# Performance work log

Measured on AMD Instinct MI355X. Metric: run time of the kernel, lower is better.

The kernel has to match this reference:

```python
import jax, jax.numpy as jnp
import numpy as np

D_MODEL = 1024
NHEAD = 16
HEAD_DIM = D_MODEL // NHEAD
EPS = 1e-5


def layer_norm(x, gamma, beta):
    mu = jnp.mean(x, axis=-1, keepdims=True)
    var = jnp.mean(jnp.square(x - mu), axis=-1, keepdims=True)
    return (x - mu) * jax.lax.rsqrt(var + EPS) * gamma + beta


def setup_inputs() -> dict:
    key = jax.random.key(0)
    ks = jax.random.split(key, 12)
    d = D_MODEL
    s = 1.0 / np.sqrt(d)
    return {
        "x": jax.random.normal(ks[0], (4, 2048, d), dtype=jnp.float32),
        "wq": jax.random.normal(ks[1], (d, d), dtype=jnp.float32) * s,
        "wk": jax.random.normal(ks[2], (d, d), dtype=jnp.float32) * s,
        "wv": jax.random.normal(ks[3], (d, d), dtype=jnp.float32) * s,
        "wo": jax.random.normal(ks[4], (d, d), dtype=jnp.float32) * s,
        "bo": jnp.zeros((d,), dtype=jnp.float32),
        "gx": jnp.ones((d,), dtype=jnp.float32),
        "bx": jnp.zeros((d,), dtype=jnp.float32),
        "gf": jnp.ones((d,), dtype=jnp.float32),
        "bf": jnp.zeros((d,), dtype=jnp.float32),
        "w1": jax.random.normal(ks[5], (d, d), dtype=jnp.float32) * s,
        "b1": jnp.zeros((d,), dtype=jnp.float32),
        "w2": jax.random.normal(ks[6], (d, d), dtype=jnp.float32) * s,
        "b2": jnp.zeros((d,), dtype=jnp.float32),
    }


def reference(x, wq, wk, wv, wo, bo, gx, bx, gf, bf, w1, b1, w2, b2):
    B, S, D = x.shape
    H, Dh = NHEAD, HEAD_DIM
    xs = layer_norm(x, gx, bx)
    q = (xs @ wq).reshape(B, S, H, Dh)
    k = (xs @ wk).reshape(B, S, H, Dh)
    v = (xs @ wv).reshape(B, S, H, Dh)
    scores = jnp.einsum("bqhd,bkhd->bhqk", q, k) / jnp.sqrt(jnp.float32(Dh))
    attn = jax.nn.softmax(scores, axis=-1)  # dropout p=0 -> identity
    o = jnp.einsum("bhqk,bkhd->bqhd", attn, v).reshape(B, S, D)
    attn_out = o @ wo + bo
    xt = x + attn_out
    h = layer_norm(xt, gf, bf)
    ffn = jax.nn.relu(h @ w1 + b1) @ w2 + b2
    return xt + ffn
```

## Files before the change

### kernel.cpp

```cpp
#include <hip/hip_runtime.h>
#include <hip/hip_bf16.h>

typedef __bf16 bf16;
typedef bf16 bf16x8 __attribute__((ext_vector_type(8)));
typedef bf16 bf16x4 __attribute__((ext_vector_type(4)));
typedef float f32x4 __attribute__((ext_vector_type(4)));
typedef float f32x16 __attribute__((ext_vector_type(16)));

#define AS1 __attribute__((address_space(1)))
#define AS3 __attribute__((address_space(3)))

static constexpr int SEQ = 2048;
static constexpr int NH  = 16;
static constexpr int DH  = 64;
static constexpr float SCLQ = 0.125f * 1.44269504088896340736f;

__device__ __forceinline__ void gload16(const void* g, void* l) {
  __builtin_amdgcn_global_load_lds((const AS1 void*)g, (AS3 void*)l, 16, 0, 0);
}

__device__ __forceinline__ unsigned pk2(float a, float b) {
  union { bf16 h[2]; unsigned u; } z;
  z.h[0] = (bf16)a; z.h[1] = (bf16)b;
  return z.u;
}

__device__ __forceinline__ void plswap(unsigned &a, unsigned &b) {
  asm volatile("v_permlane32_swap_b32 %0, %1" : "+v"(a), "+v"(b));
}

#define MFMA32(d, a, b) d = __builtin_amdgcn_mfma_f32_32x32x16_bf16(a, b, d, 0, 0, 0)

__global__ __launch_bounds__(256) void prep_w(
    const float* __restrict__ w0, const float* __restrict__ w1,
    const float* __restrict__ w2, const float* __restrict__ w3,
    const float* __restrict__ w4, const float* __restrict__ w5,
    bf16* __restrict__ dst)
{
  __shared__ float tile[64][65];
  int bid = blockIdx.x;
  int wi = bid >> 8;
  int tl = bid & 255;
  int tk = (tl >> 4) << 6;
  int tn = (tl & 15) << 6;
  const float* W = w0;
  if (wi == 1) W = w1; else if (wi == 2) W = w2; else if (wi == 3) W = w3;
  else if (wi == 4) W = w4; else if (wi == 5) W = w5;
  int t = threadIdx.x;
  #pragma unroll
  for (int rep = 0; rep < 16; ++rep) {
    int idx = rep * 256 + t;
    int i = idx >> 6, j = idx & 63;
    tile[i][j] = W[(size_t)(tk + i) * 1024 + tn + j];
  }
  __syncthreads();
  bf16* out = dst + (size_t)wi * 1024 * 1024;
  #pragma unroll
  for (int rep = 0; rep < 16; ++rep) {
    int idx = rep * 256 + t;
    int i = idx >> 6, j = idx & 63;
    out[(size_t)(tn + i) * 1024 + tk + j] = (bf16)tile[j][i];
  }
}

__global__ __launch_bounds__(256) void ln_k(
    const float* __restrict__ x, const float* __restrict__ g,
    const float* __restrict__ bb, bf16* __restrict__ out)
{
  int row = blockIdx.x;
  int t = threadIdx.x;
  float4 v = ((const float4*)(x + (size_t)row * 1024))[t];
  float s  = v.x + v.y + v.z + v.w;
  float s2 = v.x * v.x + v.y * v.y + v.z * v.z + v.w * v.w;
  #pragma unroll
  for (int m = 1; m < 64; m <<= 1) { s += __shfl_xor(s, m); s2 += __shfl_xor(s2, m); }
  __shared__ float red[8];
  int w = t >> 6;
  if ((t & 63) == 0) { red[w] = s; red[4 + w] = s2; }
  __syncthreads();
  s  = red[0] + red[1] + red[2] + red[3];
  s2 = red[4] + red[5] + red[6] + red[7];
  float mu  = s * (1.0f / 1024.0f);
  float var = s2 * (1.0f / 1024.0f) - mu * mu;
  float rst = rsqrtf(var + 1e-5f);
  float4 gv = ((const float4*)g)[t];
  float4 bv = ((const float4*)bb)[t];
  bf16x4 o;
  o[0] = (bf16)((v.x - mu) * rst * gv.x + bv.x);
  o[1] = (bf16)((v.y - mu) * rst * gv.y + bv.y);
  o[2] = (bf16)((v.z - mu) * rst * gv.z + bv.z);
  o[3] = (bf16)((v.w - mu) * rst * gv.w + bv.w);
  *(bf16x4*)(out + (size_t)row * 1024 + t * 4) = o;
}

template<int EPI, int NT>
__global__ __launch_bounds__(256) void gemm_k(
    const bf16* __restrict__ A, const bf16* __restrict__ Bt,
    const float* __restrict__ bias, const float* __restrict__ res,
    float* __restrict__ outf, bf16* __restrict__ outb)
{
  __shared__ bf16 lA[128 * 64];
  __shared__ bf16 lB[128 * 64];
  int t = threadIdx.x;
  int wg = blockIdx.x;
  int swz = (wg & 7) * (NT * 8) + (wg >> 3);
  int mt = swz / NT, nt = swz % NT;
  int lane = t & 63, w = t >> 6;
  int l16 = lane & 15, lh = lane >> 4;
  int wr = w >> 1, wc = w & 1;

  f32x4 acc[4][4] = {};
  const size_t mbase = (size_t)mt * 128;
  const size_t nbase = (size_t)nt * 128;
  int u = t & 7;

  for (int ks = 0; ks < 16; ++ks) {
    int k0 = ks * 64;
    #pragma unroll
    for (int i = 0; i < 4; ++i) {
      int row = i * 32 + (t >> 3);
      int up = u ^ (row & 7);
      gload16(A  + (mbase + row) * 1024 + k0 + up * 8, lA + i * 2048 + w * 512);
      gload16(Bt + (nbase + row) * 1024 + k0 + up * 8, lB + i * 2048 + w * 512);
    }
    __syncthreads();
    #pragma unroll
    for (int kc = 0; kc < 2; ++kc) {
      bf16x8 af[4], bfr[4];
      #pragma unroll
      for (int mi = 0; mi < 4; ++mi) {
        int row = wr * 64 + mi * 16 + l16;
        af[mi] = *(const bf16x8*)(lA + row * 64 + (((kc * 4 + lh) ^ (row & 7)) * 8));
      }
      #pragma unroll
      for (int ni = 0; ni < 4; ++ni) {
        int row = wc * 64 + ni * 16 + l16;
        bfr[ni] = *(const bf16x8*)(lB + row * 64 + (((kc * 4 + lh) ^ (row & 7)) * 8));
      }
      #pragma unroll
      for (int mi = 0; mi < 4; ++mi)
        #pragma unroll
        for (int ni = 0; ni < 4; ++ni)
          acc[mi][ni] = __builtin_amdgcn_mfma_f32_16x16x32_bf16(af[mi], bfr[ni], acc[mi][ni], 0, 0, 0);
    }
    __syncthreads();
  }

  int mrow0 = mt * 128 + wr * 64;
  int ncol0 = nt * 128 + wc * 64;
  #pragma unroll
  for (int mi = 0; mi < 4; ++mi) {
    #pragma unroll
    for (int ni = 0; ni < 4; ++ni) {
      if constexpr (EPI == 0) {
        int gcol = ncol0 + ni * 16 + l16;
        int which = gcol >> 10;
        int col = gcol & 1023;
        int h = col >> 6, dh = col & 63;
        bf16* dst = outb + (size_t)which * (size_t)(4 * NH * SEQ * DH);
        if (which == 2) {
          int s0 = mrow0 + mi * 16 + lh * 4;
          int b = s0 >> 11, s = s0 & 2047;
          bf16x4 pkv;
          #pragma unroll
          for (int r = 0; r < 4; ++r) pkv[r] = (bf16)acc[mi][ni][r];
          *(bf16x4*)(dst + (((size_t)((b * NH + h) * DH + dh)) << 11) + s) = pkv;
        } else {
          #pragma unroll
          for (int r = 0; r < 4; ++r) {
            int grow = mrow0 + mi * 16 + lh * 4 + r;
            int b = grow >> 11, s = grow & 2047;
            float v = acc[mi][ni][r];
            if (which == 0) v *= SCLQ;
            dst[(((size_t)((b * NH + h) * SEQ + s)) << 6) + dh] = (bf16)v;
          }
        }
      } else {
        #pragma unroll
        for (int r = 0; r < 4; ++r) {
          int grow = mrow0 + mi * 16 + lh * 4 + r;
          int gcol = ncol0 + ni * 16 + l16;
          float v = acc[mi][ni][r];
          if constexpr (EPI == 2) {
            size_t idx = (size_t)grow * 1024 + gcol;
            outf[idx] = v + bias[gcol] + res[idx];
          } else {
            size_t idx = (size_t)grow * 1024 + gcol;
            float z = v + bias[gcol];
            outb[idx] = (bf16)(z > 0.f ? z : 0.f);
          }
        }
      }
    }
  }
}

__global__ __launch_bounds__(256, 2) void attn_k(
    const bf16* __restrict__ q, const bf16* __restrict__ kk,
    const bf16* __restrict__ vt, bf16* __restrict__ o)
{
  __shared__ bf16 lK[2][4096];
  __shared__ bf16 lV[2][4096];

  int t = threadIdx.x;
  int lane = t & 63, w = t >> 6;
  int l31 = lane & 31, hi = lane >> 5;
  int bid = blockIdx.x;
  int swz = (bid & 7) * 64 + (bid >> 3);
  int bh = swz >> 3, qt = swz & 7;
  int q0 = qt * 256 + w * 64;
  size_t bhS = (size_t)bh * SEQ;

  const bf16* qrow0 = q + (bhS + q0 + l31) * 64 + hi * 8;
  const bf16* qrow1 = qrow0 + 32 * 64;
  bf16x8 aq0[4], aq1[4];
  #pragma unroll
  for (int ks = 0; ks < 4; ++ks) {
    aq0[ks] = *(const bf16x8*)(qrow0 + ks * 16);
    aq1[ks] = *(const bf16x8*)(qrow1 + ks * 16);
  }

  int srow = t >> 3;
  int u8 = (t & 7) ^ (srow & 7);
  const bf16* kSrc = kk + (bhS + srow) * 64 + u8 * 8;
  const bf16* vSrc = vt + ((size_t)bh * 64 + srow) * SEQ + u8 * 8;

  f32x16 oa00 = {}, oa01 = {}, oa10 = {}, oa11 = {};
  float lsum0 = 0.f, lsum1 = 0.f;

  gload16(kSrc,            &lK[0][w * 512]);
  gload16(kSrc + 2048,     &lK[0][2048 + w * 512]);
  gload16(vSrc,            &lV[0][w * 512]);
  gload16(vSrc + 32 * SEQ, &lV[0][2048 + w * 512]);
  __syncthreads();

  #pragma unroll 2
  for (int kt = 0; kt < 32; ++kt) {
    const int cur = kt & 1;
    if (kt < 31) {
      const bf16* ks2 = kSrc + (size_t)(kt + 1) * 4096;
      const bf16* vs2 = vSrc + (kt + 1) * 64;
      gload16(ks2,            &lK[cur ^ 1][w * 512]);
      gload16(ks2 + 2048,     &lK[cur ^ 1][2048 + w * 512]);
      gload16(vs2,            &lV[cur ^ 1][w * 512]);
      gload16(vs2 + 32 * SEQ, &lV[cur ^ 1][2048 + w * 512]);
    }

    const bf16* bK = &lK[cur][0];
    const bf16* bV = &lV[cur][0];

    f32x16 sA0 = {}, sB0 = {}, sA1 = {}, sB1 = {};
    __builtin_amdgcn_s_setprio(1);
    #pragma unroll
    for (int ks = 0; ks < 4; ++ks) {
      int u = ((2 * ks + hi) ^ (l31 & 7)) * 8;
      bf16x8 k0 = *(const bf16x8*)(bK + l31 * 64 + u);
      bf16x8 k1 = *(const bf16x8*)(bK + (32 + l31) * 64 + u);
      MFMA32(sA0, k0, aq0[ks]);
      MFMA32(sA1, k0, aq1[ks]);
      MFMA32(sB0, k1, aq0[ks]);
      MFMA32(sB1, k1, aq1[ks]);
    }
    __builtin_amdgcn_s_setprio(0);

    unsigned cv0[4][4], cv1[4][4];
    {
      float p[32];
      #pragma unroll
      for (int i = 0; i < 16; ++i) {
        p[i]      = __builtin_amdgcn_exp2f(sA0[i]);
        p[16 + i] = __builtin_amdgcn_exp2f(sB0[i]);
      }
      float t8[8];
      #pragma unroll
      for (int i = 0; i < 8; ++i)
        t8[i] = (p[4 * i] + p[4 * i + 1]) + (p[4 * i + 2] + p[4 * i + 3]);
      lsum0 += ((t8[0] + t8[1]) + (t8[2] + t8[3])) + ((t8[4] + t8[5]) + (t8[6] + t8[7]));
      #pragma unroll
      for (int ks = 0; ks < 4; ++ks) {
        int g = 8 * ks;
        unsigned X0 = pk2(p[g],     p[g + 1]), X1 = pk2(p[g + 2], p[g + 3]);
        unsigned Y0 = pk2(p[g + 4], p[g + 5]), Y1 = pk2(p[g + 6], p[g + 7]);
        plswap(X0, Y0);
        plswap(X1, Y1);
        cv0[ks][0] = X0; cv0[ks][1] = X1; cv0[ks][2] = Y0; cv0[ks][3] = Y1;
      }
    }
    {
      float p[32];
      #pragma unroll
      for (int i = 0; i < 16; ++i) {
        p[i]      = __builtin_amdgcn_exp2f(sA1[i]);
        p[16 + i] = __builtin_amdgcn_exp2f(sB1[i]);
      }
      float t8[8];
      #pragma unroll
      for (int i = 0; i < 8; ++i)
        t8[i] = (p[4 * i] + p[4 * i + 1]) + (p[4 * i + 2] + p[4 * i + 3]);
      lsum1 += ((t8[0] + t8[1]) + (t8[2] + t8[3])) + ((t8[4] + t8[5]) + (t8[6] + t8[7]));
      #pragma unroll
      for (int ks = 0; ks < 4; ++ks) {
        int g = 8 * ks;
        unsigned X0 = pk2(p[g],     p[g + 1]), X1 = pk2(p[g + 2], p[g + 3]);
        unsigned Y0 = pk2(p[g + 4], p[g + 5]), Y1 = pk2(p[g + 6], p[g + 7]);
        plswap(X0, Y0);
        plswap(X1, Y1);
        cv1[ks][0] = X0; cv1[ks][1] = X1; cv1[ks][2] = Y0; cv1[ks][3] = Y1;
      }
    }

    __builtin_amdgcn_s_setprio(1);
    #pragma unroll
    for (int ks = 0; ks < 4; ++ks) {
      int u = ((2 * ks + hi) ^ (l31 & 7)) * 8;
      bf16x8 v0 = *(const bf16x8*)(bV + l31 * 64 + u);
      bf16x8 v1 = *(const bf16x8*)(bV + (32 + l31) * 64 + u);
      union { unsigned u4[4]; bf16x8 v; } a0, a1;
      a0.u4[0] = cv0[ks][0]; a0.u4[1] = cv0[ks][1]; a0.u4[2] = cv0[ks][2]; a0.u4[3] = cv0[ks][3];
      a1.u4[0] = cv1[ks][0]; a1.u4[1] = cv1[ks][1]; a1.u4[2] = cv1[ks][2]; a1.u4[3] = cv1[ks][3];
      MFMA32(oa00, a0.v, v0);
      MFMA32(oa01, a0.v, v1);
      MFMA32(oa10, a1.v, v0);
      MFMA32(oa11, a1.v, v1);
    }
    __builtin_amdgcn_s_setprio(0);

    __syncthreads();
  }

  lsum0 += __shfl_xor(lsum0, 32);
  lsum1 += __shfl_xor(lsum1, 32);
  float inv0 = 1.0f / lsum0;
  float inv1 = 1.0f / lsum1;
  int bb = bh >> 4, hh = bh & 15;
  size_t obase = ((size_t)bb * SEQ + q0) * 1024 + (size_t)hh * 64;
  #pragma unroll
  for (int r = 0; r < 16; ++r) {
    int qrw = (r & 3) + 8 * (r >> 2) + 4 * hi;
    float iv0 = __shfl(inv0, qrw);
    float iv1 = __shfl(inv1, qrw);
    size_t b0 = obase + (size_t)qrw * 1024;
    size_t b1 = obase + (size_t)(32 + qrw) * 1024;
    o[b0 + l31]      = (bf16)(oa00[r] * iv0);
    o[b0 + 32 + l31] = (bf16)(oa01[r] * iv0);
    o[b1 + l31]      = (bf16)(oa10[r] * iv1);
    o[b1 + 32 + l31] = (bf16)(oa11[r] * iv1);
  }
}

extern "C" void kernel_launch(void* const* d_in, const int* in_sizes, int n_in,
                              void* d_out, int out_size, void* d_ws, size_t ws_size,
                              hipStream_t stream) {
  const float* x   = (const float*)d_in[0];
  const float* wq  = (const float*)d_in[1];
  const float* wk  = (const float*)d_in[2];
  const float* wv  = (const float*)d_in[3];
  const float* wo  = (const float*)d_in[4];
  const float* bo  = (const float*)d_in[5];
  const float* gx  = (const float*)d_in[6];
  const float* bx  = (const float*)d_in[7];
  const float* gf  = (const float*)d_in[8];
  const float* bfp = (const float*)d_in[9];
  const float* w1  = (const float*)d_in[10];
  const float* b1  = (const float*)d_in[11];
  const float* w2  = (const float*)d_in[12];
  const float* b2  = (const float*)d_in[13];

  char* ws = (char*)d_ws;
  const size_t MB = 1024 * 1024;
  bf16*  wT  = (bf16*)ws;
  bf16*  xs  = (bf16*)(ws + 12 * MB);
  bf16*  qb  = (bf16*)(ws + 28 * MB);
  bf16*  kb  = (bf16*)(ws + 44 * MB);
  bf16*  vtb = (bf16*)(ws + 60 * MB);
  bf16*  ob  = (bf16*)(ws + 12 * MB);
  float* xt  = (float*)(ws + 28 * MB);
  bf16*  hb  = (bf16*)(ws + 60 * MB);
  bf16*  a1  = (bf16*)(ws + 12 * MB);
  float* out = (float*)d_out;

  prep_w<<<1536, 256, 0, stream>>>(wq, wk, wv, wo, w1, w2, wT);
  ln_k<<<8192, 256, 0, stream>>>(x, gx, bx, xs);
  gemm_k<0, 24><<<1536, 256, 0, stream>>>(xs, wT, nullptr, nullptr, nullptr, qb);
  attn_k<<<512, 256, 0, stream>>>(qb, kb, vtb, ob);
  gemm_k<2, 8><<<512, 256, 0, stream>>>(ob, wT + (size_t)3 * MB, bo, x, xt, nullptr);
  ln_k<<<8192, 256, 0, stream>>>(xt, gf, bfp, hb);
  gemm_k<3, 8><<<512, 256, 0, stream>>>(hb, wT + (size_t)4 * MB, b1, nullptr, nullptr, a1);
  gemm_k<2, 8><<<512, 256, 0, stream>>>(a1, wT + (size_t)5 * MB, b2, xt, out, nullptr);
}
```

Baseline: 271.4 us.

## Fuse weight prep with first layernorm and store residual xt as bf16

Merges the weight transpose/convert kernel and the first layernorm into one launch, with block ranges split by blockIdx, which saves a kernel launch and lets the two independent jobs overlap. The intermediate residual xt is now stored in bf16 instead of fp32. This halves its write traffic and the reads by the second layernorm and the final GEMM epilogue. In exchange the residual path loses precision, which may raise the final output error.

Result: faster. 264.1 us (-2.7%).

```diff
diff --git a/kernel.cpp b/kernel.cpp
--- a/kernel.cpp
+++ b/kernel.cpp
@@ -31,22 +31,53 @@
 
 #define MFMA32(d, a, b) d = __builtin_amdgcn_mfma_f32_32x32x16_bf16(a, b, d, 0, 0, 0)
 
-__global__ __launch_bounds__(256) void prep_w(
+__global__ __launch_bounds__(256) void prep_ln(
     const float* __restrict__ w0, const float* __restrict__ w1,
     const float* __restrict__ w2, const float* __restrict__ w3,
     const float* __restrict__ w4, const float* __restrict__ w5,
-    bf16* __restrict__ dst)
+    bf16* __restrict__ dst,
+    const float* __restrict__ x, const float* __restrict__ g,
+    const float* __restrict__ bb, bf16* __restrict__ xs)
 {
   __shared__ float tile[64][65];
+  __shared__ float red[8];
   int bid = blockIdx.x;
-  int wi = bid >> 8;
-  int tl = bid & 255;
+  int t = threadIdx.x;
+
+  if (bid < 8192) {
+    int row = bid;
+    float4 v = ((const float4*)(x + (size_t)row * 1024))[t];
+    float s  = v.x + v.y + v.z + v.w;
+    float s2 = v.x * v.x + v.y * v.y + v.z * v.z + v.w * v.w;
+    #pragma unroll
+    for (int m = 1; m < 64; m <<= 1) { s += __shfl_xor(s, m); s2 += __shfl_xor(s2, m); }
+    int w = t >> 6;
+    if ((t & 63) == 0) { red[w] = s; red[4 + w] = s2; }
+    __syncthreads();
+    s  = red[0] + red[1] + red[2] + red[3];
+    s2 = red[4] + red[5] + red[6] + red[7];
+    float mu  = s * (1.0f / 1024.0f);
+    float var = s2 * (1.0f / 1024.0f) - mu * mu;
+    float rst = rsqrtf(var + 1e-5f);
+    float4 gv = ((const float4*)g)[t];
+    float4 bv = ((const float4*)bb)[t];
+    bf16x4 o;
+    o[0] = (bf16)((v.x - mu) * rst * gv.x + bv.x);
+    o[1] = (bf16)((v.y - mu) * rst * gv.y + bv.y);
+    o[2] = (bf16)((v.z - mu) * rst * gv.z + bv.z);
+    o[3] = (bf16)((v.w - mu) * rst * gv.w + bv.w);
+    *(bf16x4*)(xs + (size_t)row * 1024 + t * 4) = o;
+    return;
+  }
+
+  int pb = bid - 8192;
+  int wi = pb >> 8;
+  int tl = pb & 255;
   int tk = (tl >> 4) << 6;
   int tn = (tl & 15) << 6;
   const float* W = w0;
   if (wi == 1) W = w1; else if (wi == 2) W = w2; else if (wi == 3) W = w3;
   else if (wi == 4) W = w4; else if (wi == 5) W = w5;
-  int t = threadIdx.x;
   #pragma unroll
   for (int rep = 0; rep < 16; ++rep) {
     int idx = rep * 256 + t;
@@ -63,13 +94,20 @@
   }
 }
 
+template<int BF>
 __global__ __launch_bounds__(256) void ln_k(
-    const float* __restrict__ x, const float* __restrict__ g,
+    const void* __restrict__ xin, const float* __restrict__ g,
     const float* __restrict__ bb, bf16* __restrict__ out)
 {
   int row = blockIdx.x;
   int t = threadIdx.x;
-  float4 v = ((const float4*)(x + (size_t)row * 1024))[t];
+  float4 v;
+  if constexpr (BF) {
+    bf16x4 h = ((const bf16x4*)((const bf16*)xin + (size_t)row * 1024))[t];
+    v.x = (float)h[0]; v.y = (float)h[1]; v.z = (float)h[2]; v.w = (float)h[3];
+  } else {
+    v = ((const float4*)((const float*)xin + (size_t)row * 1024))[t];
+  }
   float s  = v.x + v.y + v.z + v.w;
   float s2 = v.x * v.x + v.y * v.y + v.z * v.z + v.w * v.w;
   #pragma unroll
@@ -96,7 +134,8 @@
 template<int EPI, int NT>
 __global__ __launch_bounds__(256) void gemm_k(
     const bf16* __restrict__ A, const bf16* __restrict__ Bt,
-    const float* __restrict__ bias, const float* __restrict__ res,
+    const float* __restrict__ bias, const float* __restrict__ resf,
+    const bf16* __restrict__ resb,
     float* __restrict__ outf, bf16* __restrict__ outb)
 {
   __shared__ bf16 lA[128 * 64];
@@ -181,13 +220,14 @@
           int grow = mrow0 + mi * 16 + lh * 4 + r;
           int gcol = ncol0 + ni * 16 + l16;
           float v = acc[mi][ni][r];
+          size_t idx = (size_t)grow * 1024 + gcol;
           if constexpr (EPI == 2) {
-            size_t idx = (size_t)grow * 1024 + gcol;
-            outf[idx] = v + bias[gcol] + res[idx];
-          } else {
-            size_t idx = (size_t)grow * 1024 + gcol;
+            outb[idx] = (bf16)(v + bias[gcol] + resf[idx]);
+          } else if constexpr (EPI == 3) {
             float z = v + bias[gcol];
             outb[idx] = (bf16)(z > 0.f ? z : 0.f);
+          } else {
+            outf[idx] = v + bias[gcol] + (float)resb[idx];
           }
         }
       }
@@ -374,17 +414,16 @@
   bf16*  kb  = (bf16*)(ws + 44 * MB);
   bf16*  vtb = (bf16*)(ws + 60 * MB);
   bf16*  ob  = (bf16*)(ws + 12 * MB);
-  float* xt  = (float*)(ws + 28 * MB);
+  bf16*  xtb = (bf16*)(ws + 28 * MB);
   bf16*  hb  = (bf16*)(ws + 60 * MB);
   bf16*  a1  = (bf16*)(ws + 12 * MB);
   float* out = (float*)d_out;
 
-  prep_w<<<1536, 256, 0, stream>>>(wq, wk, wv, wo, w1, w2, wT);
-  ln_k<<<8192, 256, 0, stream>>>(x, gx, bx, xs);
-  gemm_k<0, 24><<<1536, 256, 0, stream>>>(xs, wT, nullptr, nullptr, nullptr, qb);
+  prep_ln<<<9728, 256, 0, stream>>>(wq, wk, wv, wo, w1, w2, wT, x, gx, bx, xs);
+  gemm_k<0, 24><<<1536, 256, 0, stream>>>(xs, wT, nullptr, nullptr, nullptr, nullptr, qb);
   attn_k<<<512, 256, 0, stream>>>(qb, kb, vtb, ob);
-  gemm_k<2, 8><<<512, 256, 0, stream>>>(ob, wT + (size_t)3 * MB, bo, x, xt, nullptr);
-  ln_k<<<8192, 256, 0, stream>>>(xt, gf, bfp, hb);
-  gemm_k<3, 8><<<512, 256, 0, stream>>>(hb, wT + (size_t)4 * MB, b1, nullptr, nullptr, a1);
-  gemm_k<2, 8><<<512, 256, 0, stream>>>(a1, wT + (size_t)5 * MB, b2, xt, out, nullptr);
-}
+  gemm_k<2, 8><<<512, 256, 0, stream>>>(ob, wT + (size_t)3 * MB, bo, x, nullptr, nullptr, xtb);
+  ln_k<1><<<8192, 256, 0, stream>>>(xtb, gf, bfp, hb);
+  gemm_k<3, 8><<<512, 256, 0, stream>>>(hb, wT + (size_t)4 * MB, b1, nullptr, nullptr, nullptr, a1);
+  gemm_k<4, 8><<<512, 256, 0, stream>>>(a1, wT + (size_t)5 * MB, b2, nullptr, xtb, out, nullptr);
+}
```
